# Optimization experiments

Measured on AMD Instinct MI355X. Metric: run time of the kernel, lower is better.

Reference implementation:

```python
import jax, jax.numpy as jnp
import numpy as np
from jax import lax

B, S, M, D, NQ = 128, 100, 50, 128, 10000


def _xavier(key, shape):
    fan_in, fan_out = shape[0], shape[-1]
    limit = float(np.sqrt(6.0 / (fan_in + fan_out)))
    return jax.random.uniform(key, shape, jnp.float32, -limit, limit)


def setup_inputs() -> dict:
    key = jax.random.key(0)
    ks = jax.random.split(key, 16)
    return {
        "question_seq": jax.random.randint(ks[0], (B, S), 0, NQ),
        "answer_seq": jax.random.randint(ks[1], (B, S), 0, 2),
        "emb": _xavier(ks[2], (NQ, D)),
        "key_matrix": _xavier(ks[3], (M, D)),
        "vu_w1": _xavier(ks[4], (2 * D, D)),
        "vu_b1": jnp.zeros((D,), jnp.float32),
        "vu_w2": _xavier(ks[5], (D, D)),
        "vu_b2": jnp.zeros((D,), jnp.float32),
        "er_w": _xavier(ks[6], (D, D)),
        "er_b": jnp.zeros((D,), jnp.float32),
        "ad_w": _xavier(ks[7], (D, D)),
        "ad_b": jnp.zeros((D,), jnp.float32),
        "out_w1": _xavier(ks[8], (2 * D, D)),
        "out_b1": jnp.zeros((D,), jnp.float32),
        "out_w2": _xavier(ks[9], (D, 1)),
        "out_b2": jnp.zeros((1,), jnp.float32),
    }


def reference(question_seq, answer_seq, emb, key_matrix,
              vu_w1, vu_b1, vu_w2, vu_b2,
              er_w, er_b, ad_w, ad_b,
              out_w1, out_b1, out_w2, out_b2):
    # q_embed for all steps: [B,S,D]; attention over memory slots: [B,S,M]
    q_emb = emb[question_seq]
    attn = jax.nn.softmax(jnp.einsum('bsd,md->bsm', q_emb, key_matrix), axis=-1)

    def step(v, inp):
        w, qe = inp                                   # w: [B,M], qe: [B,D]
        read = jnp.einsum('bm,bmd->bd', w, v)         # attention read
        u = jnp.concatenate([read, qe], axis=-1)      # [B,2D]
        h = jnp.tanh(u @ vu_w1 + vu_b1)
        up = h @ vu_w2 + vu_b2                        # update vector [B,D]
        e = jax.nn.sigmoid(up @ er_w + er_b)          # erase gate
        a = jnp.tanh(up @ ad_w + ad_b)                # add vector
        v = v * (1.0 - w[:, :, None] * e[:, None, :]) + w[:, :, None] * a[:, None, :]
        return v, None

    v0 = jnp.zeros((B, M, D), q_emb.dtype)
    vT, _ = lax.scan(step, v0, (attn.transpose(1, 0, 2), q_emb.transpose(1, 0, 2)))

    # predict with last question (target_question=None branch)
    last_qe = q_emb[:, -1]                            # [B,D]
    last_w = attn[:, -1]                              # [B,M]
    read = jnp.einsum('bm,bmd->bd', last_w, vT)
    p_in = jnp.concatenate([read, last_qe], axis=-1)
    h = jax.nn.relu(p_in @ out_w1 + out_b1)
    pred = jax.nn.sigmoid(h @ out_w2 + out_b2)[:, 0]  # [B]
    return pred
```

## Files before the change

### kernel.cpp

```cpp
#include <hip/hip_runtime.h>

#define BB 128
#define SS 100
#define MM 50
#define DD 128
#define KROW 66

typedef float f32x2 __attribute__((ext_vector_type(2)));

#if defined(__has_builtin)
#  if __has_builtin(__builtin_elementwise_fma)
#    define HAVE_PKFMA 1
#  endif
#  if __has_builtin(__builtin_amdgcn_update_dpp)
#    define HAVE_DPP 1
#  endif
#  if __has_builtin(__builtin_amdgcn_rcpf)
#    define HAVE_RCP 1
#  endif
#endif

__device__ __forceinline__ f32x2 pkfma(f32x2 a, f32x2 b, f32x2 c) {
#ifdef HAVE_PKFMA
    return __builtin_elementwise_fma(a, b, c);
#else
    f32x2 r; r.x = fmaf(a.x, b.x, c.x); r.y = fmaf(a.y, b.y, c.y); return r;
#endif
}

__device__ __forceinline__ float qbf_add(float x) {
#ifdef HAVE_DPP
    union { float f; int i; } c, o;
    c.f = x;
    o.i = __builtin_amdgcn_update_dpp(0, c.i, 0xB1, 0xF, 0xF, true);
    x += o.f;
    c.f = x;
    o.i = __builtin_amdgcn_update_dpp(0, c.i, 0x4E, 0xF, 0xF, true);
    return x + o.f;
#else
    x += __shfl_xor(x, 1);
    x += __shfl_xor(x, 2);
    return x;
#endif
}

__device__ __forceinline__ void barrier_lgkm() {
    asm volatile("s_waitcnt lgkmcnt(0)" ::: "memory");
    __builtin_amdgcn_s_barrier();
    __builtin_amdgcn_sched_barrier(0);
}

__device__ __forceinline__ float bf2f(unsigned short u) {
    union { unsigned int i; float f; } c; c.i = ((unsigned int)u) << 16; return c.f;
}
__device__ __forceinline__ float bfu_lo(unsigned int u) {
    union { unsigned int i; float f; } c; c.i = u << 16; return c.f;
}
__device__ __forceinline__ float bfu_hi(unsigned int u) {
    union { unsigned int i; float f; } c; c.i = u & 0xffff0000u; return c.f;
}
__device__ __forceinline__ unsigned short f2bf_bits(float f) {
    union { float f; unsigned int u; } c; c.f = f;
    unsigned int r = (c.u + 0x7FFFu + ((c.u >> 16) & 1u)) >> 16;
    return (unsigned short)r;
}
__device__ __forceinline__ unsigned int packbf(float lo, float hi) {
    return (unsigned int)f2bf_bits(lo) | ((unsigned int)f2bf_bits(hi) << 16);
}
__device__ __forceinline__ float fast_rcp(float x) {
#ifdef HAVE_RCP
    return __builtin_amdgcn_rcpf(x);
#else
    return 1.0f / x;
#endif
}
__device__ __forceinline__ float fast_sigmoid(float x) {
    return fast_rcp(1.0f + __expf(-x));
}
__device__ __forceinline__ float fast_tanh(float x) {
    float ax = fabsf(x);
    float z = __expf(-2.0f * ax);
    float r = (1.0f - z) * fast_rcp(1.0f + z);
    return copysignf(r, x);
}

template <bool BF16>
__device__ __forceinline__ float ldw(const void* p, size_t idx) {
    if (BF16) return bf2f(((const unsigned short*)p)[idx]);
    return ((const float*)p)[idx];
}

__device__ __forceinline__ bool detect_bf16(const void* emb) {
    const unsigned int* eu = (const unsigned int*)emb;
    int cnt = 0;
    for (int i = 0; i < 32; ++i) {
        unsigned int e8 = (eu[i] >> 7) & 0xFFu;
        cnt += (e8 >= 100u && e8 <= 127u) ? 1 : 0;
    }
    return cnt >= 16;
}

#define W2ROW(r) ((r) * 68 + (((r) >> 5) << 3))

#define WS_WROW_OFF 0u
#define WS_QP_OFF   (BB * SS * 32u * 4u)
#define WS_W2EA_OFF (WS_QP_OFF + BB * SS * DD * 2u)
#define WS_EAB_OFF  (WS_W2EA_OFF + DD * DD * 8u)
#define WS_NEED     (WS_EAB_OFF + DD * 8u)

struct __align__(16) SmemA {
    union {
        struct {
            unsigned int key_w[MM * KROW];
            unsigned int qe8[8][68];
        } pre;
        unsigned int w2s[8724];
    } u;
};

template <bool BF16>
__device__ void pre_impl(const int* qseq, const void* emb, const void* key,
                         const void* vu_w1, unsigned int* wrow_g, unsigned short* qp_g,
                         SmemA& sm)
{
    const int t = threadIdx.x;
    const int b = blockIdx.x;
    const int half = blockIdx.y;
    const int l = t & 63;
    const int wv = t >> 6;
    const int q = l & 3;
    const int d = (wv << 4) + (l >> 2);

    if (BF16) {
        const unsigned int* kg = (const unsigned int*)key;
        for (int g = t; g < MM * 64; g += 512)
            sm.u.pre.key_w[(g >> 6) * KROW + (g & 63)] = kg[g];
    } else {
        const float* kf = (const float*)key;
        for (int g = t; g < MM * 64; g += 512) {
            int row = g >> 6, c2 = g & 63;
            sm.u.pre.key_w[row * KROW + c2] = packbf(kf[row * 128 + 2 * c2], kf[row * 128 + 2 * c2 + 1]);
        }
    }

    float rw1b[32];
#pragma unroll
    for (int i = 0; i < 32; ++i)
        rw1b[i] = ldw<BF16>(vu_w1, (size_t)(DD + 32 * q + i) * DD + d);
    __syncthreads();

    for (int ii = 0; ii < 7; ++ii) {
        const int nrows = (ii == 6) ? 2 : 8;
        {
            int r = t >> 6, w = t & 63;
            if (r < nrows) {
                int s = 50 * half + 8 * ii + r;
                int row = qseq[b * SS + s];
                if (BF16) {
                    sm.u.pre.qe8[r][w] = ((const unsigned int*)emb)[((size_t)row << 6) + w];
                } else {
                    const float* ef = (const float*)emb + (((size_t)row) << 7) + 2 * w;
                    sm.u.pre.qe8[r][w] = packbf(ef[0], ef[1]);
                }
            }
        }
        __syncthreads();

        if (wv < nrows) {
            int m = l;
            int mc = (m < MM) ? m : (MM - 1);
            float a0 = 0.f, a1 = 0.f, a2 = 0.f, a3 = 0.f;
#pragma unroll
            for (int j = 0; j < 32; ++j) {
                uint2 kw = *(const uint2*)&sm.u.pre.key_w[mc * KROW + 2 * j];
                uint2 qw = *(const uint2*)&sm.u.pre.qe8[wv][2 * j];
                a0 = fmaf(bfu_lo(kw.x), bfu_lo(qw.x), a0);
                a1 = fmaf(bfu_hi(kw.x), bfu_hi(qw.x), a1);
                a2 = fmaf(bfu_lo(kw.y), bfu_lo(qw.y), a2);
                a3 = fmaf(bfu_hi(kw.y), bfu_hi(qw.y), a3);
            }
            float lg = (a0 + a1) + (a2 + a3);
            if (m >= MM) lg = -1e30f;
            float mx = lg;
#pragma unroll
            for (int o = 32; o > 0; o >>= 1) mx = fmaxf(mx, __shfl_xor(mx, o));
            float p = (m < MM) ? __expf(lg - mx) : 0.f;
            float sum = p;
#pragma unroll
            for (int o = 32; o > 0; o >>= 1) sum += __shfl_xor(sum, o);
            p = p * fast_rcp(sum);
            float pn = __shfl_xor(p, 4);
            int s = 50 * half + 8 * ii + wv;
            if ((m & 4) == 0)
                wrow_g[(size_t)(b * SS + s) * 32 + (m & 3) * 8 + (m >> 3)] = packbf(p, pn);
        }

        for (int sr = 0; sr < nrows; ++sr) {
            float p0 = 0.f, p1 = 0.f;
#pragma unroll
            for (int i = 0; i < 16; ++i) {
                unsigned int uw = sm.u.pre.qe8[sr][16 * q + i];
                p0 = fmaf(rw1b[2 * i],     bfu_lo(uw), p0);
                p1 = fmaf(rw1b[2 * i + 1], bfu_hi(uw), p1);
            }
            float qpv = qbf_add(p0 + p1);
            int s = 50 * half + 8 * ii + sr;
            if (q == 0) qp_g[(size_t)(b * SS + s) * DD + d] = f2bf_bits(qpv);
        }
        __syncthreads();
    }
}

template <bool BF16>
__device__ void build_impl(const void* vu_w2, const void* vu_b2,
                           const void* er_w, const void* er_b,
                           const void* ad_w, const void* ad_b,
                           f32x2* w2ea_g, f32x2* eab_g, SmemA& sm)
{
    const int t = threadIdx.x;
    const int l = t & 63;
    const int wv = t >> 6;
    const int q = l & 3;
    const int d = (wv << 4) + (l >> 2);

    if (BF16) {
        const unsigned int* wg = (const unsigned int*)vu_w2;
        for (int g = t; g < 128 * 64; g += 512)
            sm.u.w2s[W2ROW(g >> 6) + (g & 63)] = wg[g];
    } else {
        const float* wf = (const float*)vu_w2;
        for (int g = t; g < 128 * 64; g += 512) {
            int row = g >> 6, c2 = g & 63;
            sm.u.w2s[W2ROW(row) + c2] = packbf(wf[row * 128 + 2 * c2], wf[row * 128 + 2 * c2 + 1]);
        }
    }
    __syncthreads();

    f32x2 rw2ea[32];
#pragma unroll
    for (int k = 0; k < 32; ++k) { rw2ea[k].x = 0.f; rw2ea[k].y = 0.f; }
    f32x2 eab2; eab2.x = 0.f; eab2.y = 0.f;
#pragma unroll 1
    for (int jc = 0; jc < 4; ++jc) {
        f32x2 ea[32];
#pragma unroll
        for (int i = 0; i < 32; ++i) {
            int j = 32 * jc + i;
            ea[i].x = ldw<BF16>(er_w, (size_t)j * DD + d);
            ea[i].y = ldw<BF16>(ad_w, (size_t)j * DD + d);
            float b2j = ldw<BF16>(vu_b2, j);
            f32x2 bs; bs.x = b2j; bs.y = b2j;
            eab2 = pkfma(bs, ea[i], eab2);
        }
#pragma unroll
        for (int k = 0; k < 32; ++k) {
            const uint4* wp = (const uint4*)&sm.u.w2s[W2ROW(32 * q + k) + 16 * jc];
            uint4 A = wp[0], B = wp[1], C = wp[2], Dv = wp[3];
            unsigned int W[16] = { A.x, A.y, A.z, A.w, B.x, B.y, B.z, B.w,
                                   C.x, C.y, C.z, C.w, Dv.x, Dv.y, Dv.z, Dv.w };
            f32x2 acc = rw2ea[k];
#pragma unroll
            for (int wd = 0; wd < 16; ++wd) {
                float wlo = bfu_lo(W[wd]), whi = bfu_hi(W[wd]);
                f32x2 s0; s0.x = wlo; s0.y = wlo;
                f32x2 s1; s1.x = whi; s1.y = whi;
                acc = pkfma(s0, ea[2 * wd], acc);
                acc = pkfma(s1, ea[2 * wd + 1], acc);
            }
            rw2ea[k] = acc;
        }
    }
    eab2.x += ldw<BF16>(er_b, d);
    eab2.y += ldw<BF16>(ad_b, d);

#pragma unroll
    for (int k = 0; k < 32; ++k)
        w2ea_g[(size_t)(32 * q + k) * DD + d] = rw2ea[k];
    if (q == 0) eab_g[d] = eab2;
}

__global__ __launch_bounds__(512) void DKVMN_78546361909953_pre(
    const int* __restrict__ qseq,
    const void* emb, const void* key, const void* vu_w1,
    const void* vu_w2, const void* vu_b2,
    const void* er_w, const void* er_b, const void* ad_w, const void* ad_b,
    void* ws)
{
    __shared__ SmemA sm;
    unsigned int*   wrow_g = (unsigned int*)((char*)ws + WS_WROW_OFF);
    unsigned short* qp_g   = (unsigned short*)((char*)ws + WS_QP_OFF);
    f32x2*          w2ea_g = (f32x2*)((char*)ws + WS_W2EA_OFF);
    f32x2*          eab_g  = (f32x2*)((char*)ws + WS_EAB_OFF);
    bool isbf = detect_bf16(emb);
    if (blockIdx.x < BB) {
        if (isbf) pre_impl<true>(qseq, emb, key, vu_w1, wrow_g, qp_g, sm);
        else      pre_impl<false>(qseq, emb, key, vu_w1, wrow_g, qp_g, sm);
    } else if (blockIdx.y == 0) {
        if (isbf) build_impl<true>(vu_w2, vu_b2, er_w, er_b, ad_w, ad_b, w2ea_g, eab_g, sm);
        else      build_impl<false>(vu_w2, vu_b2, er_w, er_b, ad_w, ad_b, w2ea_g, eab_g, sm);
    }
}

struct __align__(16) SmemB {
    float xread[152];
    float xh[152];
    float h1f[DD];
    float qlast[DD];
    unsigned int   wtab[SS][32];
    unsigned short qptab[SS][DD];
};

template <bool BF16>
__device__ void scan_impl(
    const int* __restrict__ qseq,
    const void* emb, const void* vu_w1, const void* vu_b1,
    const void* out_w1, const void* out_b1, const void* out_w2, const void* out_b2,
    const unsigned int* wrow_g, const unsigned short* qp_g,
    const f32x2* w2ea_g, const f32x2* eab_g,
    void* outp, SmemB& sm)
{
    const int t = threadIdx.x;
    const int b = blockIdx.x;
    const int l = t & 63;
    const int q = l & 3;
    const int d = ((t >> 6) << 4) + (l >> 2);

    {
        const uint4* srcw = (const uint4*)(wrow_g + (size_t)b * SS * 32);
        uint4* dstw = (uint4*)&sm.wtab[0][0];
        for (int g = t; g < SS * 32 / 4; g += 512) dstw[g] = srcw[g];
        const uint4* srcq = (const uint4*)(qp_g + (size_t)b * SS * DD);
        uint4* dstq = (uint4*)&sm.qptab[0][0];
        for (int g = t; g < SS * DD / 8; g += 512) dstq[g] = srcq[g];
    }

    if (t < 64) {
        int row = qseq[b * SS + (SS - 1)];
        if (BF16) {
            unsigned int uw = ((const unsigned int*)emb)[((size_t)row << 6) + t];
            sm.qlast[2 * t]     = bfu_lo(uw);
            sm.qlast[2 * t + 1] = bfu_hi(uw);
        } else {
            const float* ef = (const float*)emb + (((size_t)row) << 7) + 2 * t;
            sm.qlast[2 * t]     = ef[0];
            sm.qlast[2 * t + 1] = ef[1];
        }
    }

    f32x2 rw1a2[16];
#pragma unroll
    for (int i = 0; i < 16; ++i) {
        int k0 = 32 * q + 2 * i;
        rw1a2[i].x = ldw<BF16>(vu_w1, (size_t)k0 * DD + d);
        rw1a2[i].y = ldw<BF16>(vu_w1, (size_t)(k0 + 1) * DD + d);
    }
    const float b1r = ldw<BF16>(vu_b1, d);

    f32x2 rwe2[16], rwa2[16];
#pragma unroll
    for (int i = 0; i < 16; ++i) {
        f32x2 w0 = w2ea_g[(size_t)(32 * q + 2 * i) * DD + d];
        f32x2 w1 = w2ea_g[(size_t)(32 * q + 2 * i + 1) * DD + d];
        rwe2[i].x = w0.x; rwe2[i].y = w1.x;
        rwa2[i].x = w0.y; rwa2[i].y = w1.y;
    }
    const f32x2 eab2 = eab_g[d];

    f32x2 v2[7];
#pragma unroll
    for (int p = 0; p < 7; ++p) { v2[p].x = 0.f; v2[p].y = 0.f; }

    if (t < 152) sm.xread[t] = 0.f;
    __syncthreads();

    f32x2 wr2[7];
    {
        uint4 w0 = *(const uint4*)&sm.wtab[0][q * 8];
        uint4 w1 = *(const uint4*)&sm.wtab[0][q * 8 + 4];
        unsigned int ww[8] = { w0.x, w0.y, w0.z, w0.w, w1.x, w1.y, w1.z, w1.w };
#pragma unroll
        for (int p = 0; p < 7; ++p) { wr2[p].x = bfu_lo(ww[p]); wr2[p].y = bfu_hi(ww[p]); }
    }
    unsigned short qpcur = sm.qptab[0][d];

    for (int s = 0; s < SS; ++s) {
        uint4 pwA, pwB;
        unsigned short pq = 0;
        const bool hasnext = (s + 1 < SS);
        if (hasnext) {
            pwA = *(const uint4*)&sm.wtab[s + 1][q * 8];
            pwB = *(const uint4*)&sm.wtab[s + 1][q * 8 + 4];
            pq  = sm.qptab[s + 1][d];
        }

        {
            float hb = bf2f(qpcur) + b1r;
            const float4* xp = (const float4*)&sm.xread[40 * q];
            f32x2 acc0, acc1, acc2, acc3;
            acc0.x = 0.f; acc0.y = 0.f; acc1.x = 0.f; acc1.y = 0.f;
            acc2.x = 0.f; acc2.y = 0.f; acc3.x = 0.f; acc3.y = 0.f;
#pragma unroll
            for (int j = 0; j < 4; ++j) {
                float4 X = xp[2 * j];
                float4 Y = xp[2 * j + 1];
                f32x2 x01; x01.x = X.x; x01.y = X.y;
                f32x2 x23; x23.x = X.z; x23.y = X.w;
                f32x2 y01; y01.x = Y.x; y01.y = Y.y;
                f32x2 y23; y23.x = Y.z; y23.y = Y.w;
                acc0 = pkfma(rw1a2[4 * j],     x01, acc0);
                acc1 = pkfma(rw1a2[4 * j + 1], x23, acc1);
                acc2 = pkfma(rw1a2[4 * j + 2], y01, acc2);
                acc3 = pkfma(rw1a2[4 * j + 3], y23, acc3);
            }
            f32x2 ap = (acc0 + acc1) + (acc2 + acc3);
            float acc = qbf_add(ap.x + ap.y);
            float hh = fast_tanh(acc + hb);
            if (q == 0) sm.xh[d + 8 * (d >> 5)] = hh;
        }
        barrier_lgkm();

        {
            const float4* xp = (const float4*)&sm.xh[40 * q];
            f32x2 ae0, ae1, ae2, ae3, aa0, aa1, aa2, aa3;
            ae0.x = 0.f; ae0.y = 0.f; ae1.x = 0.f; ae1.y = 0.f;
            ae2.x = 0.f; ae2.y = 0.f; ae3.x = 0.f; ae3.y = 0.f;
            aa0.x = 0.f; aa0.y = 0.f; aa1.x = 0.f; aa1.y = 0.f;
            aa2.x = 0.f; aa2.y = 0.f; aa3.x = 0.f; aa3.y = 0.f;
#pragma unroll
            for (int j = 0; j < 4; ++j) {
                float4 X = xp[2 * j];
                float4 Y = xp[2 * j + 1];
                f32x2 h01; h01.x = X.x; h01.y = X.y;
                f32x2 h23; h23.x = X.z; h23.y = X.w;
                f32x2 h45; h45.x = Y.x; h45.y = Y.y;
                f32x2 h67; h67.x = Y.z; h67.y = Y.w;
                ae0 = pkfma(rwe2[4 * j],     h01, ae0);
                aa0 = pkfma(rwa2[4 * j],     h01, aa0);
                ae1 = pkfma(rwe2[4 * j + 1], h23, ae1);
                aa1 = pkfma(rwa2[4 * j + 1], h23, aa1);
                ae2 = pkfma(rwe2[4 * j + 2], h45, ae2);
                aa2 = pkfma(rwa2[4 * j + 2], h45, aa2);
                ae3 = pkfma(rwe2[4 * j + 3], h67, ae3);
                aa3 = pkfma(rwa2[4 * j + 3], h67, aa3);
            }
            f32x2 aep = (ae0 + ae1) + (ae2 + ae3);
            f32x2 aap = (aa0 + aa1) + (aa2 + aa3);
            float ae = qbf_add(aep.x + aep.y);
            float aa = qbf_add(aap.x + aap.y);
            float e = fast_sigmoid(ae + eab2.x);
            float a = fast_tanh(aa + eab2.y);
            f32x2 me; me.x = -e; me.y = -e;
            f32x2 av; av.x = a;  av.y = a;
#pragma unroll
            for (int p = 0; p < 7; ++p)
                v2[p] = pkfma(wr2[p], pkfma(me, v2[p], av), v2[p]);
            if (hasnext) {
                unsigned int ww[8] = { pwA.x, pwA.y, pwA.z, pwA.w, pwB.x, pwB.y, pwB.z, pwB.w };
#pragma unroll
                for (int p = 0; p < 7; ++p) { wr2[p].x = bfu_lo(ww[p]); wr2[p].y = bfu_hi(ww[p]); }
                qpcur = pq;
            }
            f32x2 rA; rA.x = 0.f; rA.y = 0.f;
            f32x2 rB; rB.x = 0.f; rB.y = 0.f;
            rA = pkfma(wr2[0], v2[0], rA); rB = pkfma(wr2[1], v2[1], rB);
            rA = pkfma(wr2[2], v2[2], rA); rB = pkfma(wr2[3], v2[3], rB);
            rA = pkfma(wr2[4], v2[4], rA); rB = pkfma(wr2[5], v2[5], rB);
            rA = pkfma(wr2[6], v2[6], rA);
            float rr = qbf_add((rA.x + rB.x) + (rA.y + rB.y));
            if (q == 0) sm.xread[rr == rr ? (d + 8 * (d >> 5)) : 0] = rr;
        }
        barrier_lgkm();
    }

    float acc = 0.f;
    {
        const float4* xp = (const float4*)&sm.xread[40 * q];
        const float4* qp4 = (const float4*)&sm.qlast[32 * q];
#pragma unroll
        for (int j = 0; j < 8; ++j) {
            float4 xv = xp[j];
            float4 qv = qp4[j];
            int k = 32 * q + 4 * j;
            acc = fmaf(ldw<BF16>(out_w1, (size_t)k * DD + d),       xv.x, acc);
            acc = fmaf(ldw<BF16>(out_w1, (size_t)(k + 1) * DD + d), xv.y, acc);
            acc = fmaf(ldw<BF16>(out_w1, (size_t)(k + 2) * DD + d), xv.z, acc);
            acc = fmaf(ldw<BF16>(out_w1, (size_t)(k + 3) * DD + d), xv.w, acc);
            acc = fmaf(ldw<BF16>(out_w1, (size_t)(DD + k) * DD + d),     qv.x, acc);
            acc = fmaf(ldw<BF16>(out_w1, (size_t)(DD + k + 1) * DD + d), qv.y, acc);
            acc = fmaf(ldw<BF16>(out_w1, (size_t)(DD + k + 2) * DD + d), qv.z, acc);
            acc = fmaf(ldw<BF16>(out_w1, (size_t)(DD + k + 3) * DD + d), qv.w, acc);
        }
    }
    acc = qbf_add(acc);
    float h1 = fmaxf(acc + ldw<BF16>(out_b1, d), 0.f);
    if (q == 0) sm.h1f[d] = h1;
    __syncthreads();

    if (t < 64) {
        float xs = fmaf(sm.h1f[t], ldw<BF16>(out_w2, t),
                        sm.h1f[64 + t] * ldw<BF16>(out_w2, 64 + t));
#pragma unroll
        for (int o = 32; o > 0; o >>= 1) xs += __shfl_xor(xs, o);
        if (t == 0) {
            float pred = fast_sigmoid(xs + ldw<BF16>(out_b2, 0));
            if (BF16) ((unsigned short*)outp)[b] = f2bf_bits(pred);
            else      ((float*)outp)[b] = pred;
        }
    }
}

__global__ __launch_bounds__(512) void DKVMN_78546361909953_scan(
    const int* __restrict__ qseq,
    const void* emb, const void* vu_w1, const void* vu_b1,
    const void* out_w1, const void* out_b1, const void* out_w2, const void* out_b2,
    void* ws, void* outp)
{
    __shared__ SmemB sm;
    const unsigned int*   wrow_g = (const unsigned int*)((char*)ws + WS_WROW_OFF);
    const unsigned short* qp_g   = (const unsigned short*)((char*)ws + WS_QP_OFF);
    const f32x2*          w2ea_g = (const f32x2*)((char*)ws + WS_W2EA_OFF);
    const f32x2*          eab_g  = (const f32x2*)((char*)ws + WS_EAB_OFF);
    if (detect_bf16(emb))
        scan_impl<true>(qseq, emb, vu_w1, vu_b1, out_w1, out_b1, out_w2, out_b2,
                        wrow_g, qp_g, w2ea_g, eab_g, outp, sm);
    else
        scan_impl<false>(qseq, emb, vu_w1, vu_b1, out_w1, out_b1, out_w2, out_b2,
                         wrow_g, qp_g, w2ea_g, eab_g, outp, sm);
}

struct __align__(16) SmemM {
    union {
        struct {
            unsigned int key_w[MM * KROW];
            unsigned int qe8[8][68];
        } pre;
        struct {
            float xread[152];
            float xhdup[312];
            float h1f[DD];
        } run;
    } u;
    union {
        unsigned int w2s[8724];
        struct {
            unsigned int wrow_p[SS][32];
            unsigned short qp_all[SS][DD];
        } tab;
    } v2;
    int qrow[SS];
    float qlast[DD];
};

template <bool BF16>
__device__ void mono_impl(
    const int* __restrict__ qseq,
    const void* emb, const void* key,
    const void* vu_w1, const void* vu_b1, const void* vu_w2, const void* vu_b2,
    const void* er_w, const void* er_b, const void* ad_w, const void* ad_b,
    const void* out_w1, const void* out_b1, const void* out_w2, const void* out_b2,
    void* outp, SmemM& sm)
{
    const int t = threadIdx.x;
    const int b = blockIdx.x;
    const int l = t & 63;
    const int wv = t >> 6;
    const int q = l & 3;
    const int d = (wv << 4) + (l >> 2);

    if (BF16) {
        const unsigned int* kg = (const unsigned int*)key;
        for (int g = t; g < MM * 64; g += 512)
            sm.u.pre.key_w[(g >> 6) * KROW + (g & 63)] = kg[g];
        const unsigned int* wg = (const unsigned int*)vu_w2;
        for (int g = t; g < 128 * 64; g += 512)
            sm.v2.w2s[W2ROW(g >> 6) + (g & 63)] = wg[g];
    } else {
        const float* kf = (const float*)key;
        for (int g = t; g < MM * 64; g += 512) {
            int row = g >> 6, c2 = g & 63;
            sm.u.pre.key_w[row * KROW + c2] = packbf(kf[row * 128 + 2 * c2], kf[row * 128 + 2 * c2 + 1]);
        }
        const float* wf = (const float*)vu_w2;
        for (int g = t; g < 128 * 64; g += 512) {
            int row = g >> 6, c2 = g & 63;
            sm.v2.w2s[W2ROW(row) + c2] = packbf(wf[row * 128 + 2 * c2], wf[row * 128 + 2 * c2 + 1]);
        }
    }
    for (int g = t; g < SS; g += 512) sm.qrow[g] = qseq[b * SS + g];
    __syncthreads();

    f32x2 rw2ea[32];
#pragma unroll
    for (int k = 0; k < 32; ++k) { rw2ea[k].x = 0.f; rw2ea[k].y = 0.f; }
    f32x2 eab2; eab2.x = 0.f; eab2.y = 0.f;
#pragma unroll 1
    for (int jc = 0; jc < 4; ++jc) {
        f32x2 ea[32];
#pragma unroll
        for (int i = 0; i < 32; ++i) {
            int j = 32 * jc + i;
            ea[i].x = ldw<BF16>(er_w, (size_t)j * DD + d);
            ea[i].y = ldw<BF16>(ad_w, (size_t)j * DD + d);
            float b2j = ldw<BF16>(vu_b2, j);
            f32x2 bs; bs.x = b2j; bs.y = b2j;
            eab2 = pkfma(bs, ea[i], eab2);
        }
#pragma unroll
        for (int k = 0; k < 32; ++k) {
            const uint4* wp = (const uint4*)&sm.v2.w2s[W2ROW(32 * q + k) + 16 * jc];
            uint4 A = wp[0], B = wp[1], C = wp[2], Dv = wp[3];
            unsigned int W[16] = { A.x, A.y, A.z, A.w, B.x, B.y, B.z, B.w,
                                   C.x, C.y, C.z, C.w, Dv.x, Dv.y, Dv.z, Dv.w };
            f32x2 acc = rw2ea[k];
#pragma unroll
            for (int wd = 0; wd < 16; ++wd) {
                float wlo = bfu_lo(W[wd]), whi = bfu_hi(W[wd]);
                f32x2 s0; s0.x = wlo; s0.y = wlo;
                f32x2 s1; s1.x = whi; s1.y = whi;
                acc = pkfma(s0, ea[2 * wd], acc);
                acc = pkfma(s1, ea[2 * wd + 1], acc);
            }
            rw2ea[k] = acc;
        }
    }
    eab2.x += ldw<BF16>(er_b, d);
    eab2.y += ldw<BF16>(ad_b, d);
    __syncthreads();

    float rw1a[32], rw1b[32];
#pragma unroll
    for (int i = 0; i < 32; ++i) {
        rw1a[i] = ldw<BF16>(vu_w1, (size_t)(32 * q + i) * DD + d);
        rw1b[i] = ldw<BF16>(vu_w1, (size_t)(DD + 32 * q + i) * DD + d);
    }
    const float b1r = ldw<BF16>(vu_b1, d);

    for (int ii = 0; ii < 13; ++ii) {
        const int nrows = (ii == 12) ? 4 : 8;
        {
            int r = t >> 6, w = t & 63;
            if (r < nrows) {
                int row = sm.qrow[8 * ii + r];
                if (BF16) {
                    sm.u.pre.qe8[r][w] = ((const unsigned int*)emb)[((size_t)row << 6) + w];
                } else {
                    const float* ef = (const float*)emb + (((size_t)row) << 7) + 2 * w;
                    sm.u.pre.qe8[r][w] = packbf(ef[0], ef[1]);
                }
            }
        }
        __syncthreads();

        if (wv < nrows) {
            int m = l;
            int mc = (m < MM) ? m : (MM - 1);
            float a0 = 0.f, a1 = 0.f, a2 = 0.f, a3 = 0.f;
#pragma unroll
            for (int j = 0; j < 32; ++j) {
                uint2 kw = *(const uint2*)&sm.u.pre.key_w[mc * KROW + 2 * j];
                uint2 qw = *(const uint2*)&sm.u.pre.qe8[wv][2 * j];
                a0 = fmaf(bfu_lo(kw.x), bfu_lo(qw.x), a0);
                a1 = fmaf(bfu_hi(kw.x), bfu_hi(qw.x), a1);
                a2 = fmaf(bfu_lo(kw.y), bfu_lo(qw.y), a2);
                a3 = fmaf(bfu_hi(kw.y), bfu_hi(qw.y), a3);
            }
            float lg = (a0 + a1) + (a2 + a3);
            if (m >= MM) lg = -1e30f;
            float mx = lg;
#pragma unroll
            for (int o = 32; o > 0; o >>= 1) mx = fmaxf(mx, __shfl_xor(mx, o));
            float p = (m < MM) ? __expf(lg - mx) : 0.f;
            float sum = p;
#pragma unroll
            for (int o = 32; o > 0; o >>= 1) sum += __shfl_xor(sum, o);
            p = p * fast_rcp(sum);
            float pn = __shfl_xor(p, 4);
            if ((m & 4) == 0)
                sm.v2.tab.wrow_p[8 * ii + wv][(m & 3) * 8 + (m >> 3)] = packbf(p, pn);
        }

        for (int sr = 0; sr < nrows; ++sr) {
            float p0 = 0.f, p1 = 0.f;
#pragma unroll
            for (int i = 0; i < 16; ++i) {
                unsigned int uw = sm.u.pre.qe8[sr][16 * q + i];
                p0 = fmaf(rw1b[2 * i],     bfu_lo(uw), p0);
                p1 = fmaf(rw1b[2 * i + 1], bfu_hi(uw), p1);
            }
            float qpv = qbf_add(p0 + p1);
            if (q == 0) sm.v2.tab.qp_all[8 * ii + sr][d] = f2bf_bits(qpv);
        }
        __syncthreads();
    }

    if (t < 64) {
        unsigned int uw = sm.u.pre.qe8[3][t];
        sm.qlast[2 * t]     = bfu_lo(uw);
        sm.qlast[2 * t + 1] = bfu_hi(uw);
    }
    f32x2 v2[7];
#pragma unroll
    for (int p = 0; p < 7; ++p) { v2[p].x = 0.f; v2[p].y = 0.f; }
    f32x2 wr2[7];
    {
        const uint4* wp = (const uint4*)&sm.v2.tab.wrow_p[0][q * 8];
        uint4 w0 = wp[0], w1 = wp[1];
        unsigned int ww[8] = { w0.x, w0.y, w0.z, w0.w, w1.x, w1.y, w1.z, w1.w };
#pragma unroll
        for (int p = 0; p < 7; ++p) { wr2[p].x = bfu_lo(ww[p]); wr2[p].y = bfu_hi(ww[p]); }
    }
    if (t < 152) sm.u.run.xread[t] = 0.f;
    __syncthreads();

    for (int s = 0; s < SS; ++s) {
        {
            float qpv = bf2f(sm.v2.tab.qp_all[s][d]);
            const float4* xp = (const float4*)&sm.u.run.xread[40 * q];
            f32x2 rw1a2_j;
            f32x2 acc2; acc2.x = 0.f; acc2.y = 0.f;
#pragma unroll
            for (int j = 0; j < 8; ++j) {
                float4 X = xp[j];
                f32x2 x01; x01.x = X.x; x01.y = X.y;
                f32x2 x23; x23.x = X.z; x23.y = X.w;
                rw1a2_j.x = rw1a[4 * j];     rw1a2_j.y = rw1a[4 * j + 1];
                acc2 = pkfma(rw1a2_j, x01, acc2);
                rw1a2_j.x = rw1a[4 * j + 2]; rw1a2_j.y = rw1a[4 * j + 3];
                acc2 = pkfma(rw1a2_j, x23, acc2);
            }
            float acc = qbf_add(acc2.x + acc2.y);
            float hh = fast_tanh(acc + qpv + b1r);
            if (q == 0) {
                f32x2 hd; hd.x = hh; hd.y = hh;
                *(f32x2*)&sm.u.run.xhdup[2 * d + 8 * ((2 * d) >> 5)] = hd;
            }
        }
        __syncthreads();

        {
            f32x2 acc2; acc2.x = 0.f; acc2.y = 0.f;
#pragma unroll
            for (int blk = 0; blk < 2; ++blk) {
                const float4* xp = (const float4*)&sm.u.run.xhdup[80 * q + 40 * blk];
#pragma unroll
                for (int j = 0; j < 8; ++j) {
                    float4 X = xp[j];
                    f32x2 s0; s0.x = X.x; s0.y = X.y;
                    f32x2 s1; s1.x = X.z; s1.y = X.w;
                    int k = 16 * blk + 2 * j;
                    acc2 = pkfma(rw2ea[k], s0, acc2);
                    acc2 = pkfma(rw2ea[k + 1], s1, acc2);
                }
            }
            float ae = qbf_add(acc2.x);
            float aa = qbf_add(acc2.y);
            float e = fast_sigmoid(ae + eab2.x);
            float a = fast_tanh(aa + eab2.y);
            f32x2 me; me.x = -e; me.y = -e;
            f32x2 av; av.x = a;  av.y = a;
#pragma unroll
            for (int p = 0; p < 7; ++p)
                v2[p] = pkfma(wr2[p], pkfma(me, v2[p], av), v2[p]);
            if (s + 1 < SS) {
                const uint4* wp = (const uint4*)&sm.v2.tab.wrow_p[s + 1][q * 8];
                uint4 w0 = wp[0], w1 = wp[1];
                unsigned int ww[8] = { w0.x, w0.y, w0.z, w0.w, w1.x, w1.y, w1.z, w1.w };
#pragma unroll
                for (int p = 0; p < 7; ++p) { wr2[p].x = bfu_lo(ww[p]); wr2[p].y = bfu_hi(ww[p]); }
            }
            f32x2 racc; racc.x = 0.f; racc.y = 0.f;
#pragma unroll
            for (int p = 0; p < 7; ++p)
                racc = pkfma(wr2[p], v2[p], racc);
            float rr = qbf_add(racc.x + racc.y);
            if (q == 0) sm.u.run.xread[d + 8 * (d >> 5)] = rr;
        }
        __syncthreads();
    }

    float acc = 0.f;
    {
        const float4* xp = (const float4*)&sm.u.run.xread[40 * q];
        const float4* qp4 = (const float4*)&sm.qlast[32 * q];
#pragma unroll
        for (int j = 0; j < 8; ++j) {
            float4 xv = xp[j];
            float4 qv = qp4[j];
            int k = 32 * q + 4 * j;
            acc = fmaf(ldw<BF16>(out_w1, (size_t)k * DD + d),       xv.x, acc);
            acc = fmaf(ldw<BF16>(out_w1, (size_t)(k + 1) * DD + d), xv.y, acc);
            acc = fmaf(ldw<BF16>(out_w1, (size_t)(k + 2) * DD + d), xv.z, acc);
            acc = fmaf(ldw<BF16>(out_w1, (size_t)(k + 3) * DD + d), xv.w, acc);
            acc = fmaf(ldw<BF16>(out_w1, (size_t)(DD + k) * DD + d),     qv.x, acc);
            acc = fmaf(ldw<BF16>(out_w1, (size_t)(DD + k + 1) * DD + d), qv.y, acc);
            acc = fmaf(ldw<BF16>(out_w1, (size_t)(DD + k + 2) * DD + d), qv.z, acc);
            acc = fmaf(ldw<BF16>(out_w1, (size_t)(DD + k + 3) * DD + d), qv.w, acc);
        }
    }
    acc = qbf_add(acc);
    float h1 = fmaxf(acc + ldw<BF16>(out_b1, d), 0.f);
    if (q == 0) sm.u.run.h1f[d] = h1;
    __syncthreads();

    if (t < 64) {
        float xs = fmaf(sm.u.run.h1f[t], ldw<BF16>(out_w2, t),
                        sm.u.run.h1f[64 + t] * ldw<BF16>(out_w2, 64 + t));
#pragma unroll
        for (int o = 32; o > 0; o >>= 1) xs += __shfl_xor(xs, o);
        if (t == 0) {
            float pred = fast_sigmoid(xs + ldw<BF16>(out_b2, 0));
            if (BF16) ((unsigned short*)outp)[b] = f2bf_bits(pred);
            else      ((float*)outp)[b] = pred;
        }
    }
}

__global__ __launch_bounds__(512) void DKVMN_78546361909953_kernel(
    const int* __restrict__ qseq,
    const void* emb, const void* key,
    const void* vu_w1, const void* vu_b1, const void* vu_w2, const void* vu_b2,
    const void* er_w, const void* er_b, const void* ad_w, const void* ad_b,
    const void* out_w1, const void* out_b1, const void* out_w2, const void* out_b2,
    void* outp)
{
    __shared__ SmemM sm;
    if (detect_bf16(emb))
        mono_impl<true>(qseq, emb, key, vu_w1, vu_b1, vu_w2, vu_b2,
                        er_w, er_b, ad_w, ad_b, out_w1, out_b1, out_w2, out_b2, outp, sm);
    else
        mono_impl<false>(qseq, emb, key, vu_w1, vu_b1, vu_w2, vu_b2,
                         er_w, er_b, ad_w, ad_b, out_w1, out_b1, out_w2, out_b2, outp, sm);
}

extern "C" void kernel_launch(void* const* d_in, const int* in_sizes, int n_in,
                              void* d_out, int out_size, void* d_ws, size_t ws_size,
                              hipStream_t stream) {
    const int* qseq = (const int*)d_in[0];
    if (ws_size >= (size_t)WS_NEED) {
        DKVMN_78546361909953_pre<<<dim3(BB + 1, 2), 512, 0, stream>>>(
            qseq, d_in[2], d_in[3], d_in[4],
            d_in[6], d_in[7], d_in[8], d_in[9], d_in[10], d_in[11], d_ws);
        DKVMN_78546361909953_scan<<<BB, 512, 0, stream>>>(
            qseq, d_in[2], d_in[4], d_in[5],
            d_in[12], d_in[13], d_in[14], d_in[15], d_ws, d_out);
    } else {
        DKVMN_78546361909953_kernel<<<BB, 512, 0, stream>>>(
            qseq, d_in[2], d_in[3], d_in[4], d_in[5], d_in[6], d_in[7],
            d_in[8], d_in[9], d_in[10], d_in[11],
            d_in[12], d_in[13], d_in[14], d_in[15], d_out);
    }
}
```

Measured before the change: 247.0 us.

## Precompute next-step read algebraically to take memory update off the critical path

The next step's attention read is rewritten as r1 - e*r2 + a*c, where r1, r2 and c are dot products of the current and next weights with the memory. These are computed before the erase/add gates are known, so after the gates only a few FMAs separate the gates from the read written to shared memory. The memory update itself now runs after that write. Biases are folded into the accumulator initial values, shared-memory operands are loaded up front into register arrays, and launch bounds request 2 blocks per SM. This adds extra FMAs per step and more register pressure, and drops the NaN guard on the read store.

```diff
diff --git a/kernel.cpp b/kernel.cpp
--- a/kernel.cpp
+++ b/kernel.cpp
@@ -384,56 +384,84 @@
     unsigned short qpcur = sm.qptab[0][d];
 
     for (int s = 0; s < SS; ++s) {
-        uint4 pwA, pwB;
-        unsigned short pq = 0;
         const bool hasnext = (s + 1 < SS);
+
+        const float4* xp = (const float4*)&sm.xread[40 * q];
+        float4 X[8];
+#pragma unroll
+        for (int j = 0; j < 8; ++j) X[j] = xp[j];
+
+        f32x2 wr2n[7];
+        unsigned short pq = qpcur;
         if (hasnext) {
-            pwA = *(const uint4*)&sm.wtab[s + 1][q * 8];
-            pwB = *(const uint4*)&sm.wtab[s + 1][q * 8 + 4];
-            pq  = sm.qptab[s + 1][d];
-        }
+            uint4 pwA = *(const uint4*)&sm.wtab[s + 1][q * 8];
+            uint4 pwB = *(const uint4*)&sm.wtab[s + 1][q * 8 + 4];
+            pq = sm.qptab[s + 1][d];
+            unsigned int ww[8] = { pwA.x, pwA.y, pwA.z, pwA.w, pwB.x, pwB.y, pwB.z, pwB.w };
+#pragma unroll
+            for (int p = 0; p < 7; ++p) { wr2n[p].x = bfu_lo(ww[p]); wr2n[p].y = bfu_hi(ww[p]); }
+        } else {
+#pragma unroll
+            for (int p = 0; p < 7; ++p) wr2n[p] = wr2[p];
+        }
+        float hb = bf2f(qpcur) + b1r;
+
+        f32x2 cA; cA.x = 0.f; cA.y = 0.f;
+        f32x2 r1A; r1A.x = 0.f; r1A.y = 0.f;
+        f32x2 r2A; r2A.x = 0.f; r2A.y = 0.f;
+#pragma unroll
+        for (int p = 0; p < 7; ++p) {
+            f32x2 wn = wr2n[p];
+            f32x2 wnw = wn * wr2[p];
+            cA  = pkfma(wn,  wr2[p], cA);
+            r1A = pkfma(wn,  v2[p],  r1A);
+            r2A = pkfma(wnw, v2[p],  r2A);
+        }
+        float cfull = qbf_add(cA.x + cA.y);
+        float r1    = qbf_add(r1A.x + r1A.y);
+        float r2    = qbf_add(r2A.x + r2A.y);
 
         {
-            float hb = bf2f(qpcur) + b1r;
-            const float4* xp = (const float4*)&sm.xread[40 * q];
             f32x2 acc0, acc1, acc2, acc3;
-            acc0.x = 0.f; acc0.y = 0.f; acc1.x = 0.f; acc1.y = 0.f;
-            acc2.x = 0.f; acc2.y = 0.f; acc3.x = 0.f; acc3.y = 0.f;
+            acc0.x = hb * 0.25f; acc0.y = 0.f;
+            acc1.x = 0.f; acc1.y = 0.f;
+            acc2.x = 0.f; acc2.y = 0.f;
+            acc3.x = 0.f; acc3.y = 0.f;
 #pragma unroll
             for (int j = 0; j < 4; ++j) {
-                float4 X = xp[2 * j];
-                float4 Y = xp[2 * j + 1];
-                f32x2 x01; x01.x = X.x; x01.y = X.y;
-                f32x2 x23; x23.x = X.z; x23.y = X.w;
-                f32x2 y01; y01.x = Y.x; y01.y = Y.y;
-                f32x2 y23; y23.x = Y.z; y23.y = Y.w;
+                f32x2 x01; x01.x = X[2 * j].x;     x01.y = X[2 * j].y;
+                f32x2 x23; x23.x = X[2 * j].z;     x23.y = X[2 * j].w;
+                f32x2 y01; y01.x = X[2 * j + 1].x; y01.y = X[2 * j + 1].y;
+                f32x2 y23; y23.x = X[2 * j + 1].z; y23.y = X[2 * j + 1].w;
                 acc0 = pkfma(rw1a2[4 * j],     x01, acc0);
                 acc1 = pkfma(rw1a2[4 * j + 1], x23, acc1);
                 acc2 = pkfma(rw1a2[4 * j + 2], y01, acc2);
                 acc3 = pkfma(rw1a2[4 * j + 3], y23, acc3);
             }
             f32x2 ap = (acc0 + acc1) + (acc2 + acc3);
-            float acc = qbf_add(ap.x + ap.y);
-            float hh = fast_tanh(acc + hb);
+            float u = qbf_add(ap.x + ap.y);
+            float hh = fast_tanh(u);
             if (q == 0) sm.xh[d + 8 * (d >> 5)] = hh;
         }
         barrier_lgkm();
 
         {
-            const float4* xp = (const float4*)&sm.xh[40 * q];
+            const float4* hp = (const float4*)&sm.xh[40 * q];
+            float4 H[8];
+#pragma unroll
+            for (int j = 0; j < 8; ++j) H[j] = hp[j];
+
             f32x2 ae0, ae1, ae2, ae3, aa0, aa1, aa2, aa3;
-            ae0.x = 0.f; ae0.y = 0.f; ae1.x = 0.f; ae1.y = 0.f;
-            ae2.x = 0.f; ae2.y = 0.f; ae3.x = 0.f; ae3.y = 0.f;
-            aa0.x = 0.f; aa0.y = 0.f; aa1.x = 0.f; aa1.y = 0.f;
-            aa2.x = 0.f; aa2.y = 0.f; aa3.x = 0.f; aa3.y = 0.f;
+            ae0.x = eab2.x * 0.25f; ae0.y = 0.f;
+            ae1.x = 0.f; ae1.y = 0.f; ae2.x = 0.f; ae2.y = 0.f; ae3.x = 0.f; ae3.y = 0.f;
+            aa0.x = eab2.y * 0.25f; aa0.y = 0.f;
+            aa1.x = 0.f; aa1.y = 0.f; aa2.x = 0.f; aa2.y = 0.f; aa3.x = 0.f; aa3.y = 0.f;
 #pragma unroll
             for (int j = 0; j < 4; ++j) {
-                float4 X = xp[2 * j];
-                float4 Y = xp[2 * j + 1];
-                f32x2 h01; h01.x = X.x; h01.y = X.y;
-                f32x2 h23; h23.x = X.z; h23.y = X.w;
-                f32x2 h45; h45.x = Y.x; h45.y = Y.y;
-                f32x2 h67; h67.x = Y.z; h67.y = Y.w;
+                f32x2 h01; h01.x = H[2 * j].x;     h01.y = H[2 * j].y;
+                f32x2 h23; h23.x = H[2 * j].z;     h23.y = H[2 * j].w;
+                f32x2 h45; h45.x = H[2 * j + 1].x; h45.y = H[2 * j + 1].y;
+                f32x2 h67; h67.x = H[2 * j + 1].z; h67.y = H[2 * j + 1].w;
                 ae0 = pkfma(rwe2[4 * j],     h01, ae0);
                 aa0 = pkfma(rwa2[4 * j],     h01, aa0);
                 ae1 = pkfma(rwe2[4 * j + 1], h23, ae1);
@@ -447,27 +475,22 @@
             f32x2 aap = (aa0 + aa1) + (aa2 + aa3);
             float ae = qbf_add(aep.x + aep.y);
             float aa = qbf_add(aap.x + aap.y);
-            float e = fast_sigmoid(ae + eab2.x);
-            float a = fast_tanh(aa + eab2.y);
-            f32x2 me; me.x = -e; me.y = -e;
-            f32x2 av; av.x = a;  av.y = a;
-#pragma unroll
-            for (int p = 0; p < 7; ++p)
-                v2[p] = pkfma(wr2[p], pkfma(me, v2[p], av), v2[p]);
+            float e = fast_sigmoid(ae);
+            float a = fast_tanh(aa);
+
+            float rr = fmaf(cfull, a, fmaf(-e, r2, r1));
+            if (q == 0) sm.xread[d + 8 * (d >> 5)] = rr;
+
             if (hasnext) {
-                unsigned int ww[8] = { pwA.x, pwA.y, pwA.z, pwA.w, pwB.x, pwB.y, pwB.z, pwB.w };
-#pragma unroll
-                for (int p = 0; p < 7; ++p) { wr2[p].x = bfu_lo(ww[p]); wr2[p].y = bfu_hi(ww[p]); }
+                f32x2 me; me.x = -e; me.y = -e;
+                f32x2 av; av.x = a;  av.y = a;
+#pragma unroll
+                for (int p = 0; p < 7; ++p)
+                    v2[p] = pkfma(wr2[p], pkfma(me, v2[p], av), v2[p]);
+#pragma unroll
+                for (int p = 0; p < 7; ++p) wr2[p] = wr2n[p];
                 qpcur = pq;
             }
-            f32x2 rA; rA.x = 0.f; rA.y = 0.f;
-            f32x2 rB; rB.x = 0.f; rB.y = 0.f;
-            rA = pkfma(wr2[0], v2[0], rA); rB = pkfma(wr2[1], v2[1], rB);
-            rA = pkfma(wr2[2], v2[2], rA); rB = pkfma(wr2[3], v2[3], rB);
-            rA = pkfma(wr2[4], v2[4], rA); rB = pkfma(wr2[5], v2[5], rB);
-            rA = pkfma(wr2[6], v2[6], rA);
-            float rr = qbf_add((rA.x + rB.x) + (rA.y + rB.y));
-            if (q == 0) sm.xread[rr == rr ? (d + 8 * (d >> 5)) : 0] = rr;
         }
         barrier_lgkm();
     }
@@ -509,7 +532,7 @@
     }
 }
 
-__global__ __launch_bounds__(512) void DKVMN_78546361909953_scan(
+__global__ __launch_bounds__(512, 2) void DKVMN_78546361909953_scan(
     const int* __restrict__ qseq,
     const void* emb, const void* vu_w1, const void* vu_b1,
     const void* out_w1, const void* out_b1, const void* out_w2, const void* out_b2,
```

Result: no change. 250.9 us (+1.6%).

## Use bf16 dot2 instructions for per-step matvecs with packed bf16 weights

Applied to the files above, without the earlier changes.

Packs the vu_w1, erase and add weight registers into bf16 pairs and uses v_dot2_f32_bf16 for the per-step hidden and erase/add matvecs. The shared-memory read and hidden vectors are stored as bf16, which halves LDS traffic and register footprint. Biases are folded into the accumulator initial values, exp is replaced by exp2 with a prescaled argument, and the launch bounds ask for two blocks per CU. Intermediate activations are now rounded to bf16, which lowers precision for the fp32 path, and the NaN-guard store index is removed.

```diff
diff --git a/kernel.cpp b/kernel.cpp
--- a/kernel.cpp
+++ b/kernel.cpp
@@ -18,6 +18,15 @@
 #  if __has_builtin(__builtin_amdgcn_rcpf)
 #    define HAVE_RCP 1
 #  endif
+#  if __has_builtin(__builtin_amdgcn_exp2f)
+#    define EXP2(x) __builtin_amdgcn_exp2f(x)
+#  endif
+#  if __has_builtin(__builtin_amdgcn_fdot2_f32_bf16)
+#    define HAVE_DOT2BF 1
+#  endif
+#endif
+#ifndef EXP2
+#  define EXP2(x) exp2f(x)
 #endif
 
 __device__ __forceinline__ f32x2 pkfma(f32x2 a, f32x2 b, f32x2 c) {
@@ -75,14 +84,24 @@
 #endif
 }
 __device__ __forceinline__ float fast_sigmoid(float x) {
-    return fast_rcp(1.0f + __expf(-x));
+    return fast_rcp(1.0f + EXP2(x * -1.4426950408889634f));
 }
 __device__ __forceinline__ float fast_tanh(float x) {
     float ax = fabsf(x);
-    float z = __expf(-2.0f * ax);
+    float z = EXP2(ax * -2.8853900817779268f);
     float r = (1.0f - z) * fast_rcp(1.0f + z);
     return copysignf(r, x);
 }
+
+#ifdef HAVE_DOT2BF
+typedef __bf16 bf2v __attribute__((ext_vector_type(2)));
+__device__ __forceinline__ bf2v u2bf(unsigned int u) {
+    union { unsigned int x; bf2v v; } c; c.x = u; return c.v;
+}
+__device__ __forceinline__ float dot2bf(unsigned int a, unsigned int b, float c) {
+    return __builtin_amdgcn_fdot2_f32_bf16(u2bf(a), u2bf(b), c, false);
+}
+#endif
 
 template <bool BF16>
 __device__ __forceinline__ float ldw(const void* p, size_t idx) {
@@ -302,8 +321,13 @@
 }
 
 struct __align__(16) SmemB {
+#ifdef HAVE_DOT2BF
+    unsigned short xread[144];
+    unsigned short xh[144];
+#else
     float xread[152];
     float xh[152];
+#endif
     float h1f[DD];
     float qlast[DD];
     unsigned int   wtab[SS][32];
@@ -347,6 +371,22 @@
         }
     }
 
+    const float b1r = ldw<BF16>(vu_b1, d);
+    const f32x2 eab2 = eab_g[d];
+
+#ifdef HAVE_DOT2BF
+    unsigned int rw1p[16], rwep[16], rwap[16];
+#pragma unroll
+    for (int i = 0; i < 16; ++i) {
+        int k0 = 32 * q + 2 * i;
+        rw1p[i] = packbf(ldw<BF16>(vu_w1, (size_t)k0 * DD + d),
+                         ldw<BF16>(vu_w1, (size_t)(k0 + 1) * DD + d));
+        f32x2 w0 = w2ea_g[(size_t)k0 * DD + d];
+        f32x2 w1 = w2ea_g[(size_t)(k0 + 1) * DD + d];
+        rwep[i] = packbf(w0.x, w1.x);
+        rwap[i] = packbf(w0.y, w1.y);
+    }
+#else
     f32x2 rw1a2[16];
 #pragma unroll
     for (int i = 0; i < 16; ++i) {
@@ -354,8 +394,6 @@
         rw1a2[i].x = ldw<BF16>(vu_w1, (size_t)k0 * DD + d);
         rw1a2[i].y = ldw<BF16>(vu_w1, (size_t)(k0 + 1) * DD + d);
     }
-    const float b1r = ldw<BF16>(vu_b1, d);
-
     f32x2 rwe2[16], rwa2[16];
 #pragma unroll
     for (int i = 0; i < 16; ++i) {
@@ -364,22 +402,30 @@
         rwe2[i].x = w0.x; rwe2[i].y = w1.x;
         rwa2[i].x = w0.y; rwa2[i].y = w1.y;
     }
-    const f32x2 eab2 = eab_g[d];
+#endif
 
     f32x2 v2[7];
 #pragma unroll
     for (int p = 0; p < 7; ++p) { v2[p].x = 0.f; v2[p].y = 0.f; }
 
+#ifdef HAVE_DOT2BF
+    if (t < 144) sm.xread[t] = 0;
+#else
     if (t < 152) sm.xread[t] = 0.f;
+#endif
     __syncthreads();
 
     f32x2 wr2[7];
     {
         uint4 w0 = *(const uint4*)&sm.wtab[0][q * 8];
         uint4 w1 = *(const uint4*)&sm.wtab[0][q * 8 + 4];
-        unsigned int ww[8] = { w0.x, w0.y, w0.z, w0.w, w1.x, w1.y, w1.z, w1.w };
-#pragma unroll
-        for (int p = 0; p < 7; ++p) { wr2[p].x = bfu_lo(ww[p]); wr2[p].y = bfu_hi(ww[p]); }
+        wr2[0].x = bfu_lo(w0.x); wr2[0].y = bfu_hi(w0.x);
+        wr2[1].x = bfu_lo(w0.y); wr2[1].y = bfu_hi(w0.y);
+        wr2[2].x = bfu_lo(w0.z); wr2[2].y = bfu_hi(w0.z);
+        wr2[3].x = bfu_lo(w0.w); wr2[3].y = bfu_hi(w0.w);
+        wr2[4].x = bfu_lo(w1.x); wr2[4].y = bfu_hi(w1.x);
+        wr2[5].x = bfu_lo(w1.y); wr2[5].y = bfu_hi(w1.y);
+        wr2[6].x = bfu_lo(w1.z); wr2[6].y = bfu_hi(w1.z);
     }
     unsigned short qpcur = sm.qptab[0][d];
 
@@ -395,10 +441,35 @@
 
         {
             float hb = bf2f(qpcur) + b1r;
+#ifdef HAVE_DOT2BF
+            const uint4* xp = (const uint4*)&sm.xread[32 * q];
+            uint4 X0 = xp[0], X1 = xp[1], X2 = xp[2], X3 = xp[3];
+            float a0 = dot2bf(rw1p[0],  X0.x, hb * 0.25f);
+            float a1 = dot2bf(rw1p[1],  X0.y, 0.f);
+            float a2 = dot2bf(rw1p[2],  X0.z, 0.f);
+            float a3 = dot2bf(rw1p[3],  X0.w, 0.f);
+            a0 = dot2bf(rw1p[4],  X1.x, a0);
+            a1 = dot2bf(rw1p[5],  X1.y, a1);
+            a2 = dot2bf(rw1p[6],  X1.z, a2);
+            a3 = dot2bf(rw1p[7],  X1.w, a3);
+            a0 = dot2bf(rw1p[8],  X2.x, a0);
+            a1 = dot2bf(rw1p[9],  X2.y, a1);
+            a2 = dot2bf(rw1p[10], X2.z, a2);
+            a3 = dot2bf(rw1p[11], X2.w, a3);
+            a0 = dot2bf(rw1p[12], X3.x, a0);
+            a1 = dot2bf(rw1p[13], X3.y, a1);
+            a2 = dot2bf(rw1p[14], X3.z, a2);
+            a3 = dot2bf(rw1p[15], X3.w, a3);
+            float u = qbf_add((a0 + a1) + (a2 + a3));
+            float hh = fast_tanh(u);
+            if (q == 0) sm.xh[d] = f2bf_bits(hh);
+#else
             const float4* xp = (const float4*)&sm.xread[40 * q];
             f32x2 acc0, acc1, acc2, acc3;
-            acc0.x = 0.f; acc0.y = 0.f; acc1.x = 0.f; acc1.y = 0.f;
-            acc2.x = 0.f; acc2.y = 0.f; acc3.x = 0.f; acc3.y = 0.f;
+            acc0.x = hb * 0.25f; acc0.y = 0.f;
+            acc1.x = 0.f; acc1.y = 0.f;
+            acc2.x = 0.f; acc2.y = 0.f;
+            acc3.x = 0.f; acc3.y = 0.f;
 #pragma unroll
             for (int j = 0; j < 4; ++j) {
                 float4 X = xp[2 * j];
@@ -413,23 +484,50 @@
                 acc3 = pkfma(rw1a2[4 * j + 3], y23, acc3);
             }
             f32x2 ap = (acc0 + acc1) + (acc2 + acc3);
-            float acc = qbf_add(ap.x + ap.y);
-            float hh = fast_tanh(acc + hb);
+            float u = qbf_add(ap.x + ap.y);
+            float hh = fast_tanh(u);
             if (q == 0) sm.xh[d + 8 * (d >> 5)] = hh;
+#endif
         }
         barrier_lgkm();
 
         {
-            const float4* xp = (const float4*)&sm.xh[40 * q];
+#ifdef HAVE_DOT2BF
+            const uint4* hp = (const uint4*)&sm.xh[32 * q];
+            uint4 H0 = hp[0], H1 = hp[1], H2 = hp[2], H3 = hp[3];
+            float e0 = dot2bf(rwep[0],  H0.x, eab2.x * 0.25f);
+            float g0 = dot2bf(rwap[0],  H0.x, eab2.y * 0.25f);
+            float e1 = dot2bf(rwep[1],  H0.y, 0.f);
+            float g1 = dot2bf(rwap[1],  H0.y, 0.f);
+            float e2 = dot2bf(rwep[2],  H0.z, 0.f);
+            float g2 = dot2bf(rwap[2],  H0.z, 0.f);
+            float e3 = dot2bf(rwep[3],  H0.w, 0.f);
+            float g3 = dot2bf(rwap[3],  H0.w, 0.f);
+            e0 = dot2bf(rwep[4],  H1.x, e0);  g0 = dot2bf(rwap[4],  H1.x, g0);
+            e1 = dot2bf(rwep[5],  H1.y, e1);  g1 = dot2bf(rwap[5],  H1.y, g1);
+            e2 = dot2bf(rwep[6],  H1.z, e2);  g2 = dot2bf(rwap[6],  H1.z, g2);
+            e3 = dot2bf(rwep[7],  H1.w, e3);  g3 = dot2bf(rwap[7],  H1.w, g3);
+            e0 = dot2bf(rwep[8],  H2.x, e0);  g0 = dot2bf(rwap[8],  H2.x, g0);
+            e1 = dot2bf(rwep[9],  H2.y, e1);  g1 = dot2bf(rwap[9],  H2.y, g1);
+            e2 = dot2bf(rwep[10], H2.z, e2);  g2 = dot2bf(rwap[10], H2.z, g2);
+            e3 = dot2bf(rwep[11], H2.w, e3);  g3 = dot2bf(rwap[11], H2.w, g3);
+            e0 = dot2bf(rwep[12], H3.x, e0);  g0 = dot2bf(rwap[12], H3.x, g0);
+            e1 = dot2bf(rwep[13], H3.y, e1);  g1 = dot2bf(rwap[13], H3.y, g1);
+            e2 = dot2bf(rwep[14], H3.z, e2);  g2 = dot2bf(rwap[14], H3.z, g2);
+            e3 = dot2bf(rwep[15], H3.w, e3);  g3 = dot2bf(rwap[15], H3.w, g3);
+            float ae = qbf_add((e0 + e1) + (e2 + e3));
+            float aa = qbf_add((g0 + g1) + (g2 + g3));
+#else
+            const float4* hp = (const float4*)&sm.xh[40 * q];
             f32x2 ae0, ae1, ae2, ae3, aa0, aa1, aa2, aa3;
-            ae0.x = 0.f; ae0.y = 0.f; ae1.x = 0.f; ae1.y = 0.f;
-            ae2.x = 0.f; ae2.y = 0.f; ae3.x = 0.f; ae3.y = 0.f;
-            aa0.x = 0.f; aa0.y = 0.f; aa1.x = 0.f; aa1.y = 0.f;
-            aa2.x = 0.f; aa2.y = 0.f; aa3.x = 0.f; aa3.y = 0.f;
+            ae0.x = eab2.x * 0.25f; ae0.y = 0.f;
+            ae1.x = 0.f; ae1.y = 0.f; ae2.x = 0.f; ae2.y = 0.f; ae3.x = 0.f; ae3.y = 0.f;
+            aa0.x = eab2.y * 0.25f; aa0.y = 0.f;
+            aa1.x = 0.f; aa1.y = 0.f; aa2.x = 0.f; aa2.y = 0.f; aa3.x = 0.f; aa3.y = 0.f;
 #pragma unroll
             for (int j = 0; j < 4; ++j) {
-                float4 X = xp[2 * j];
-                float4 Y = xp[2 * j + 1];
+                float4 X = hp[2 * j];
+                float4 Y = hp[2 * j + 1];
                 f32x2 h01; h01.x = X.x; h01.y = X.y;
                 f32x2 h23; h23.x = X.z; h23.y = X.w;
                 f32x2 h45; h45.x = Y.x; h45.y = Y.y;
@@ -447,17 +545,22 @@
             f32x2 aap = (aa0 + aa1) + (aa2 + aa3);
             float ae = qbf_add(aep.x + aep.y);
             float aa = qbf_add(aap.x + aap.y);
-            float e = fast_sigmoid(ae + eab2.x);
-            float a = fast_tanh(aa + eab2.y);
-            f32x2 me; me.x = -e; me.y = -e;
-            f32x2 av; av.x = a;  av.y = a;
+#endif
+            float e = fast_sigmoid(ae);
+            float a = fast_tanh(aa);
+            f32x2 ev; ev.x = e; ev.y = e;
+            f32x2 av; av.x = a; av.y = a;
 #pragma unroll
             for (int p = 0; p < 7; ++p)
-                v2[p] = pkfma(wr2[p], pkfma(me, v2[p], av), v2[p]);
+                v2[p] = pkfma(wr2[p], pkfma(-ev, v2[p], av), v2[p]);
             if (hasnext) {
-                unsigned int ww[8] = { pwA.x, pwA.y, pwA.z, pwA.w, pwB.x, pwB.y, pwB.z, pwB.w };
-#pragma unroll
-                for (int p = 0; p < 7; ++p) { wr2[p].x = bfu_lo(ww[p]); wr2[p].y = bfu_hi(ww[p]); }
+                wr2[0].x = bfu_lo(pwA.x); wr2[0].y = bfu_hi(pwA.x);
+                wr2[1].x = bfu_lo(pwA.y); wr2[1].y = bfu_hi(pwA.y);
+                wr2[2].x = bfu_lo(pwA.z); wr2[2].y = bfu_hi(pwA.z);
+                wr2[3].x = bfu_lo(pwA.w); wr2[3].y = bfu_hi(pwA.w);
+                wr2[4].x = bfu_lo(pwB.x); wr2[4].y = bfu_hi(pwB.x);
+                wr2[5].x = bfu_lo(pwB.y); wr2[5].y = bfu_hi(pwB.y);
+                wr2[6].x = bfu_lo(pwB.z); wr2[6].y = bfu_hi(pwB.z);
                 qpcur = pq;
             }
             f32x2 rA; rA.x = 0.f; rA.y = 0.f;
@@ -467,13 +570,39 @@
             rA = pkfma(wr2[4], v2[4], rA); rB = pkfma(wr2[5], v2[5], rB);
             rA = pkfma(wr2[6], v2[6], rA);
             float rr = qbf_add((rA.x + rB.x) + (rA.y + rB.y));
-            if (q == 0) sm.xread[rr == rr ? (d + 8 * (d >> 5)) : 0] = rr;
+#ifdef HAVE_DOT2BF
+            if (q == 0) sm.xread[d] = f2bf_bits(rr);
+#else
+            if (q == 0) sm.xread[d + 8 * (d >> 5)] = rr;
+#endif
         }
         barrier_lgkm();
     }
 
     float acc = 0.f;
     {
+#ifdef HAVE_DOT2BF
+        const uint4* xw4 = (const uint4*)&sm.xread[32 * q];
+        uint4 W0 = xw4[0], W1 = xw4[1], W2 = xw4[2], W3 = xw4[3];
+        unsigned int XW[16] = { W0.x, W0.y, W0.z, W0.w, W1.x, W1.y, W1.z, W1.w,
+                                W2.x, W2.y, W2.z, W2.w, W3.x, W3.y, W3.z, W3.w };
+#pragma unroll
+        for (int i = 0; i < 16; ++i) {
+            int k = 32 * q + 2 * i;
+            acc = fmaf(ldw<BF16>(out_w1, (size_t)k * DD + d),       bfu_lo(XW[i]), acc);
+            acc = fmaf(ldw<BF16>(out_w1, (size_t)(k + 1) * DD + d), bfu_hi(XW[i]), acc);
+        }
+        const float4* qp4 = (const float4*)&sm.qlast[32 * q];
+#pragma unroll
+        for (int j = 0; j < 8; ++j) {
+            float4 qv = qp4[j];
+            int k = 32 * q + 4 * j;
+            acc = fmaf(ldw<BF16>(out_w1, (size_t)(DD + k) * DD + d),     qv.x, acc);
+            acc = fmaf(ldw<BF16>(out_w1, (size_t)(DD + k + 1) * DD + d), qv.y, acc);
+            acc = fmaf(ldw<BF16>(out_w1, (size_t)(DD + k + 2) * DD + d), qv.z, acc);
+            acc = fmaf(ldw<BF16>(out_w1, (size_t)(DD + k + 3) * DD + d), qv.w, acc);
+        }
+#else
         const float4* xp = (const float4*)&sm.xread[40 * q];
         const float4* qp4 = (const float4*)&sm.qlast[32 * q];
 #pragma unroll
@@ -490,6 +619,7 @@
             acc = fmaf(ldw<BF16>(out_w1, (size_t)(DD + k + 2) * DD + d), qv.z, acc);
             acc = fmaf(ldw<BF16>(out_w1, (size_t)(DD + k + 3) * DD + d), qv.w, acc);
         }
+#endif
     }
     acc = qbf_add(acc);
     float h1 = fmaxf(acc + ldw<BF16>(out_b1, d), 0.f);
@@ -509,7 +639,7 @@
     }
 }
 
-__global__ __launch_bounds__(512) void DKVMN_78546361909953_scan(
+__global__ __launch_bounds__(512, 2) void DKVMN_78546361909953_scan(
     const int* __restrict__ qseq,
     const void* emb, const void* vu_w1, const void* vu_b1,
     const void* out_w1, const void* out_b1, const void* out_w2, const void* out_b2,
```

Result: faster. 240.1 us (-2.8%).
